# Optimization experiments

Hardware: AMD Instinct MI355X
Metric: run time of the kernel (lower is better)

## Reference

```python
import jax, jax.numpy as jnp
import numpy as np

TEMPERATURE = 0.5
SCALE_LOSS = 1.0 / 32.0
LAMBDA = 0.0039


def setup_inputs() -> dict:
    key = jax.random.key(0)
    z = jax.random.normal(key, (4096, 6, 256), dtype=jnp.float32)
    return {"z": z}


def reference(z):
    B, V = z.shape[0], z.shape[1]
    # [B, V, ...] -> [V, B, D], L2-normalize embeddings
    zv = z.reshape(B, V, -1).transpose(1, 0, 2)
    zn = zv / jnp.linalg.norm(zv, axis=-1, keepdims=True)

    # Positive error: per-sample cross-view similarity [B, V, V]
    sim_pos = jnp.einsum('vbd,wbd->bvw', zn, zn)
    pos = jnp.exp((1.0 - sim_pos) / TEMPERATURE).mean(axis=(1, 2))  # [B]

    # Negative error: per-view within-batch similarity [V, B, B]
    sim_neg = jnp.exp(jnp.einsum('vbd,vcd->vbc', zn, zn) / TEMPERATURE)
    offdiag_mask = ~jnp.eye(B, dtype=bool)  # [B, B]
    off_mean = jnp.where(offdiag_mask[None], sim_neg, 0.0).sum(-1) / (B - 1)  # [V, B]
    neg = off_mean.sum(0)  # [B], accumulated over views

    return jnp.sum(pos) * SCALE_LOSS + LAMBDA * jnp.sum(neg)
```

## Files before the change

### kernel.cpp

```cpp
#include <hip/hip_runtime.h>
#include <cstdint>
#include <cstddef>

#define B_N 4096
#define V_N 6
#define D_N 256
#define CHUNK 8
#define NCHUNK 80
#define NNEG (NCHUNK * V_N)

typedef int i32x4 __attribute__((ext_vector_type(4)));

#define QC 298.0f
#define INV_C2_X2 (2.0f / (QC * QC))

__device__ __forceinline__ void async_load16(void* lds, const void* gmem) {
  __builtin_amdgcn_global_load_lds(
      (const __attribute__((address_space(1))) unsigned int*)gmem,
      (__attribute__((address_space(3))) unsigned int*)lds,
      16, 0, 0);
}

__global__ __launch_bounds__(256) void norm_pos_kernel(
    const float* __restrict__ z, signed char* __restrict__ znb,
    float* __restrict__ pos_part) {
  const int lane = threadIdx.x & 63;
  const int w = threadIdx.x >> 6;
  const int b = blockIdx.x * 4 + w;

  const float4* zb4 = (const float4*)(z + (size_t)b * (V_N * D_N));
  float4 x[V_N];
#pragma unroll
  for (int v = 0; v < V_N; ++v) x[v] = zb4[v * 64 + lane];

  float s[21];
  {
    int p = 0;
#pragma unroll
    for (int v = 0; v < V_N; ++v)
#pragma unroll
      for (int u = v; u < V_N; ++u) {
        s[p] = x[v].x * x[u].x + x[v].y * x[u].y +
               x[v].z * x[u].z + x[v].w * x[u].w;
        ++p;
      }
  }
#pragma unroll
  for (int off = 1; off < 64; off <<= 1)
#pragma unroll
    for (int q = 0; q < 21; ++q)
      s[q] += __shfl_xor(s[q], off);

  const int selfidx[V_N] = {0, 6, 11, 15, 18, 20};
  float inv[V_N];
#pragma unroll
  for (int v = 0; v < V_N; ++v) inv[v] = rsqrtf(s[selfidx[v]]);

#pragma unroll
  for (int v = 0; v < V_N; ++v) {
    const float sc = inv[v] * QC;
    int q0 = (int)rintf(fminf(127.0f, fmaxf(-127.0f, x[v].x * sc)));
    int q1 = (int)rintf(fminf(127.0f, fmaxf(-127.0f, x[v].y * sc)));
    int q2 = (int)rintf(fminf(127.0f, fmaxf(-127.0f, x[v].z * sc)));
    int q3 = (int)rintf(fminf(127.0f, fmaxf(-127.0f, x[v].w * sc)));
    int packed = (q0 & 255) | ((q1 & 255) << 8) | ((q2 & 255) << 16)
               | ((q3 & 255) << 24);
    ((int*)(znb + ((size_t)v * B_N + b) * D_N))[lane] = packed;
  }

  float psum = 0.0f;
  {
    int p = 0;
#pragma unroll
    for (int v = 0; v < V_N; ++v)
#pragma unroll
      for (int u = v; u < V_N; ++u) {
        if (u > v) psum += __expf(2.0f * (1.0f - s[p] * inv[v] * inv[u]));
        ++p;
      }
  }
  if (lane == 0) pos_part[b] = psum;
}

__global__ __launch_bounds__(256, 2) void gram_kernel(
    const signed char* __restrict__ znb, float* __restrict__ neg_part) {
  const int v = blockIdx.y;

  int i = 31, rem = blockIdx.x;
  for (int r = 31; r >= 0; --r) {
    const int nc = (r + 8) >> 3;
    if (rem < nc) { i = r; break; }
    rem -= nc;
  }
  const int j0 = rem * CHUNK;
  const int jend = min(j0 + CHUNK, i + 1);
  const int T = jend - j0;
  const int nsteps = 2 * T;

  const signed char* Zv = znb + (size_t)v * B_N * D_N;
  const signed char* Ag = Zv + (size_t)(i * 128) * D_N;

  __shared__ signed char As[128][256];
  __shared__ signed char Bs[2][128][128];
  __shared__ float blk[4];

  const int tid = threadIdx.x;
  const int lane = tid & 63;
  const int w = tid >> 6;
  const int wr = w >> 1;
  const int wc = w & 1;

  const int kc = lane >> 4;
  const int mrow = wr * 64 + (lane & 15);
  const int ncol = wc * 64 + (lane & 15);

  signed char* AsF = &As[0][0];

#pragma unroll
  for (int q = 0; q < 8; ++q) {
    const int sA = tid + 256 * q;
    const int row = sA >> 4;
    const int gc = (sA & 15) ^ (row & 15);
    async_load16(AsF + sA * 16, Ag + (size_t)row * D_N + gc * 16);
  }
#pragma unroll
  for (int st = 0; st < 2; ++st) {
    if (st < nsteps) {
      const int jn = j0 + (st >> 1), hn = st & 1;
      const signed char* Bg = Zv + (size_t)(jn * 128) * D_N + hn * 128;
      signed char* BsF = &Bs[st & 1][0][0];
#pragma unroll
      for (int q = 0; q < 4; ++q) {
        const int s = tid + 256 * q;
        const int row = s >> 3;
        const int gc = (s & 7) ^ (row & 7);
        async_load16(BsF + s * 16, Bg + (size_t)row * D_N + gc * 16);
      }
    }
  }
  asm volatile("s_waitcnt vmcnt(4)" ::: "memory");
  __builtin_amdgcn_sched_barrier(0);
  __builtin_amdgcn_s_barrier();

  float wsum = 0.0f;
  int s = 0;
  for (int jt = j0; jt < jend; ++jt) {
    i32x4 c[4][4];
#pragma unroll
    for (int a = 0; a < 4; ++a)
#pragma unroll
      for (int b2 = 0; b2 < 4; ++b2) c[a][b2] = (i32x4){0, 0, 0, 0};

#pragma unroll
    for (int h = 0; h < 2; ++h, ++s) {
      const signed char* BsF = &Bs[s & 1][0][0];
      __builtin_amdgcn_s_setprio(1);
#pragma unroll
      for (int kk = 0; kk < 2; ++kk) {
        const int cb8 = kk * 4 + kc;
        const int ca16 = h * 8 + kk * 4 + kc;
        i32x4 af[4], bfr[4];
#pragma unroll
        for (int f = 0; f < 4; ++f) {
          const int ra = mrow + 16 * f;
          const int rb = ncol + 16 * f;
          af[f]  = *(const i32x4*)(AsF + ra * 256 + ((ca16 ^ (ra & 15)) * 16));
          bfr[f] = *(const i32x4*)(BsF + rb * 128 + ((cb8 ^ (rb & 7)) * 16));
        }
#pragma unroll
        for (int fm = 0; fm < 4; ++fm)
#pragma unroll
          for (int fn = 0; fn < 4; ++fn)
            c[fm][fn] = __builtin_amdgcn_mfma_i32_16x16x64_i8(
                af[fm], bfr[fn], c[fm][fn], 0, 0, 0);
      }
      __builtin_amdgcn_s_setprio(0);
      __builtin_amdgcn_s_barrier();
      const int sn = s + 2;
      if (sn < nsteps) {
        const int jn = j0 + (sn >> 1), hn = sn & 1;
        const signed char* Bg = Zv + (size_t)(jn * 128) * D_N + hn * 128;
        signed char* BsN = &Bs[s & 1][0][0];
#pragma unroll
        for (int q = 0; q < 4; ++q) {
          const int sg = tid + 256 * q;
          const int row = sg >> 3;
          const int gc = (sg & 7) ^ (row & 7);
          async_load16(BsN + sg * 16, Bg + (size_t)row * D_N + gc * 16);
        }
      }
      if (h == 1) {
        float tsum = 0.0f;
        const int rb0 = i * 128 + wr * 64 + (lane >> 4) * 4;
        const int cb0 = jt * 128 + wc * 64 + (lane & 15);
#pragma unroll
        for (int fm = 0; fm < 4; ++fm)
#pragma unroll
          for (int fn = 0; fn < 4; ++fn) {
            const int gcol = cb0 + fn * 16;
#pragma unroll
            for (int r = 0; r < 4; ++r) {
              const int grow = rb0 + fm * 16 + r;
              float e = __expf((float)c[fm][fn][r] * INV_C2_X2);
              tsum += (grow == gcol) ? 0.0f : e;
            }
          }
        wsum += (i != jt) ? 2.0f * tsum : tsum;
      }
      if (sn < nsteps) {
        asm volatile("s_waitcnt vmcnt(4)" ::: "memory");
      } else {
        asm volatile("s_waitcnt vmcnt(0)" ::: "memory");
      }
      __builtin_amdgcn_sched_barrier(0);
      __builtin_amdgcn_s_barrier();
    }
  }

#pragma unroll
  for (int off = 32; off > 0; off >>= 1) wsum += __shfl_down(wsum, off);
  if (lane == 0) blk[w] = wsum;
  __syncthreads();
  if (tid == 0)
    neg_part[blockIdx.y * NCHUNK + blockIdx.x] =
        blk[0] + blk[1] + blk[2] + blk[3];
}

__global__ __launch_bounds__(1024) void finalize_kernel(
    const float* __restrict__ pos_part, const float* __restrict__ neg_part,
    float* __restrict__ out) {
  const int t = threadIdx.x;
  const int lane = t & 63;
  const int w = t >> 6;
  __shared__ float pr[16], nr[16];

  float p = 0.0f;
  for (int idx = t; idx < B_N; idx += 1024) p += pos_part[idx];
  float n = 0.0f;
  for (int idx = t; idx < NNEG; idx += 1024) n += neg_part[idx];
#pragma unroll
  for (int off = 32; off > 0; off >>= 1) {
    p += __shfl_down(p, off);
    n += __shfl_down(n, off);
  }
  if (lane == 0) { pr[w] = p; nr[w] = n; }
  __syncthreads();
  if (t == 0) {
    float P = 0.0f, N = 0.0f;
#pragma unroll
    for (int k = 0; k < 16; ++k) { P += pr[k]; N += nr[k]; }
    out[0] = (1.0f / 32.0f) * ((float)B_N / 6.0f + P / 18.0f) +
             0.0039f * (N / (float)(B_N - 1));
  }
}

extern "C" void kernel_launch(void* const* d_in, const int* in_sizes, int n_in,
                              void* d_out, int out_size, void* d_ws, size_t ws_size,
                              hipStream_t stream) {
  const float* z = (const float*)d_in[0];
  float* out = (float*)d_out;
  float* pos_part = (float*)d_ws;
  float* neg_part = (float*)((char*)d_ws + 16384);
  signed char* znb = (signed char*)((char*)d_ws + 32768);

  norm_pos_kernel<<<B_N / 4, 256, 0, stream>>>(z, znb, pos_part);
  dim3 grid(NCHUNK, V_N, 1);
  gram_kernel<<<grid, 256, 0, stream>>>(znb, neg_part);
  finalize_kernel<<<1, 1024, 0, stream>>>(pos_part, neg_part, out);
}
```

Before: 102.4 us.

## Fuse finalize reduction into gram kernel via last-block atomic counter

Removes the separate finalize kernel launch: each gram block writes its partial sum, bumps an atomic counter, and the last block to finish reduces all partials and writes the output. norm_pos now pre-reduces per block, cutting the pos partials from 4096 to 1024. The gram epilogue also splits off-diagonal tiles into a branch without the diagonal mask compare. The cost is one atomic and a threadfence per block, plus a serial tail of work in the last block.

```diff
diff --git a/kernel.cpp b/kernel.cpp
--- a/kernel.cpp
+++ b/kernel.cpp
@@ -7,7 +7,8 @@
 #define D_N 256
 #define CHUNK 8
 #define NCHUNK 80
-#define NNEG (NCHUNK * V_N)
+#define NGRAM (NCHUNK * V_N)
+#define NPOSB 1024
 
 typedef int i32x4 __attribute__((ext_vector_type(4)));
 
@@ -23,10 +24,13 @@
 
 __global__ __launch_bounds__(256) void norm_pos_kernel(
     const float* __restrict__ z, signed char* __restrict__ znb,
-    float* __restrict__ pos_part) {
+    float* __restrict__ pos_blk, int* __restrict__ done) {
   const int lane = threadIdx.x & 63;
   const int w = threadIdx.x >> 6;
   const int b = blockIdx.x * 4 + w;
+  __shared__ float red[4];
+
+  if (blockIdx.x == 0 && threadIdx.x == 0) *done = 0;
 
   const float4* zb4 = (const float4*)(z + (size_t)b * (V_N * D_N));
   float4 x[V_N];
@@ -79,12 +83,18 @@
         ++p;
       }
   }
-  if (lane == 0) pos_part[b] = psum;
+  if (lane == 0) red[w] = psum;
+  __syncthreads();
+  if (threadIdx.x == 0)
+    pos_blk[blockIdx.x] = red[0] + red[1] + red[2] + red[3];
 }
 
 __global__ __launch_bounds__(256, 2) void gram_kernel(
-    const signed char* __restrict__ znb, float* __restrict__ neg_part) {
+    const signed char* __restrict__ znb, const float* __restrict__ pos_blk,
+    float* __restrict__ neg_blk, int* __restrict__ done,
+    float* __restrict__ out) {
   const int v = blockIdx.y;
+  const int bid = blockIdx.y * NCHUNK + blockIdx.x;
 
   int i = 31, rem = blockIdx.x;
   for (int r = 31; r >= 0; --r) {
@@ -94,22 +104,21 @@
   }
   const int j0 = rem * CHUNK;
   const int jend = min(j0 + CHUNK, i + 1);
-  const int T = jend - j0;
-  const int nsteps = 2 * T;
+  const int nsteps = 2 * (jend - j0);
 
   const signed char* Zv = znb + (size_t)v * B_N * D_N;
   const signed char* Ag = Zv + (size_t)(i * 128) * D_N;
 
   __shared__ signed char As[128][256];
   __shared__ signed char Bs[2][128][128];
-  __shared__ float blk[4];
+  __shared__ float red[4];
+  __shared__ int lastblk;
 
   const int tid = threadIdx.x;
   const int lane = tid & 63;
   const int w = tid >> 6;
   const int wr = w >> 1;
   const int wc = w & 1;
-
   const int kc = lane >> 4;
   const int mrow = wr * 64 + (lane & 15);
   const int ncol = wc * 64 + (lane & 15);
@@ -191,21 +200,32 @@
       }
       if (h == 1) {
         float tsum = 0.0f;
-        const int rb0 = i * 128 + wr * 64 + (lane >> 4) * 4;
-        const int cb0 = jt * 128 + wc * 64 + (lane & 15);
-#pragma unroll
-        for (int fm = 0; fm < 4; ++fm)
-#pragma unroll
-          for (int fn = 0; fn < 4; ++fn) {
-            const int gcol = cb0 + fn * 16;
-#pragma unroll
-            for (int r = 0; r < 4; ++r) {
-              const int grow = rb0 + fm * 16 + r;
-              float e = __expf((float)c[fm][fn][r] * INV_C2_X2);
-              tsum += (grow == gcol) ? 0.0f : e;
+        if (i != jt) {
+#pragma unroll
+          for (int fm = 0; fm < 4; ++fm)
+#pragma unroll
+            for (int fn = 0; fn < 4; ++fn)
+#pragma unroll
+              for (int r = 0; r < 4; ++r)
+                tsum += __expf((float)c[fm][fn][r] * INV_C2_X2);
+          wsum += 2.0f * tsum;
+        } else {
+          const int rb0 = wr * 64 + (lane >> 4) * 4;
+          const int cb0 = wc * 64 + (lane & 15);
+#pragma unroll
+          for (int fm = 0; fm < 4; ++fm)
+#pragma unroll
+            for (int fn = 0; fn < 4; ++fn) {
+              const int gcol = cb0 + fn * 16;
+#pragma unroll
+              for (int r = 0; r < 4; ++r) {
+                const int grow = rb0 + fm * 16 + r;
+                float e = __expf((float)c[fm][fn][r] * INV_C2_X2);
+                tsum += (grow == gcol) ? 0.0f : e;
+              }
             }
-          }
-        wsum += (i != jt) ? 2.0f * tsum : tsum;
+          wsum += tsum;
+        }
       }
       if (sn < nsteps) {
         asm volatile("s_waitcnt vmcnt(4)" ::: "memory");
@@ -219,38 +239,35 @@
 
 #pragma unroll
   for (int off = 32; off > 0; off >>= 1) wsum += __shfl_down(wsum, off);
-  if (lane == 0) blk[w] = wsum;
+  if (lane == 0) red[w] = wsum;
   __syncthreads();
-  if (tid == 0)
-    neg_part[blockIdx.y * NCHUNK + blockIdx.x] =
-        blk[0] + blk[1] + blk[2] + blk[3];
-}
-
-__global__ __launch_bounds__(1024) void finalize_kernel(
-    const float* __restrict__ pos_part, const float* __restrict__ neg_part,
-    float* __restrict__ out) {
-  const int t = threadIdx.x;
-  const int lane = t & 63;
-  const int w = t >> 6;
-  __shared__ float pr[16], nr[16];
-
-  float p = 0.0f;
-  for (int idx = t; idx < B_N; idx += 1024) p += pos_part[idx];
-  float n = 0.0f;
-  for (int idx = t; idx < NNEG; idx += 1024) n += neg_part[idx];
-#pragma unroll
-  for (int off = 32; off > 0; off >>= 1) {
-    p += __shfl_down(p, off);
-    n += __shfl_down(n, off);
-  }
-  if (lane == 0) { pr[w] = p; nr[w] = n; }
+  if (tid == 0) {
+    neg_blk[bid] = red[0] + red[1] + red[2] + red[3];
+    __threadfence();
+    lastblk = (atomicAdd(done, 1) == NGRAM - 1) ? 1 : 0;
+  }
   __syncthreads();
-  if (t == 0) {
-    float P = 0.0f, N = 0.0f;
-#pragma unroll
-    for (int k = 0; k < 16; ++k) { P += pr[k]; N += nr[k]; }
-    out[0] = (1.0f / 32.0f) * ((float)B_N / 6.0f + P / 18.0f) +
-             0.0039f * (N / (float)(B_N - 1));
+
+  if (lastblk) {
+    float p = 0.0f, n = 0.0f;
+    for (int idx = tid; idx < NPOSB; idx += 256) p += pos_blk[idx];
+    for (int idx = tid; idx < NGRAM; idx += 256)
+      n += __hip_atomic_load(&neg_blk[idx], __ATOMIC_RELAXED,
+                             __HIP_MEMORY_SCOPE_AGENT);
+#pragma unroll
+    for (int off = 32; off > 0; off >>= 1) {
+      p += __shfl_down(p, off);
+      n += __shfl_down(n, off);
+    }
+    __shared__ float pr[4], nr[4];
+    if (lane == 0) { pr[w] = p; nr[w] = n; }
+    __syncthreads();
+    if (tid == 0) {
+      float P = pr[0] + pr[1] + pr[2] + pr[3];
+      float N = nr[0] + nr[1] + nr[2] + nr[3];
+      out[0] = (1.0f / 32.0f) * ((float)B_N / 6.0f + P / 18.0f) +
+               0.0039f * (N / (float)(B_N - 1));
+    }
   }
 }
 
@@ -259,12 +276,12 @@
                               hipStream_t stream) {
   const float* z = (const float*)d_in[0];
   float* out = (float*)d_out;
-  float* pos_part = (float*)d_ws;
-  float* neg_part = (float*)((char*)d_ws + 16384);
+  float* pos_blk = (float*)d_ws;
+  float* neg_blk = (float*)((char*)d_ws + 8192);
+  int* done = (int*)((char*)d_ws + 16384);
   signed char* znb = (signed char*)((char*)d_ws + 32768);
 
-  norm_pos_kernel<<<B_N / 4, 256, 0, stream>>>(z, znb, pos_part);
+  norm_pos_kernel<<<NPOSB, 256, 0, stream>>>(z, znb, pos_blk, done);
   dim3 grid(NCHUNK, V_N, 1);
-  gram_kernel<<<grid, 256, 0, stream>>>(znb, neg_part);
-  finalize_kernel<<<1, 1024, 0, stream>>>(pos_part, neg_part, out);
-}
+  gram_kernel<<<grid, 256, 0, stream>>>(znb, pos_blk, neg_blk, done, out);
+}
```

Result: slower. 108.5 us (+6.0%).
